# Optimization experiments

Hardware: AMD Instinct MI355X
Metric: run time of the kernel (lower is better)

Reference implementation:

```python
import jax, jax.numpy as jnp
import numpy as np

FEAT = 9
H = 128
L = 2
NH = 4
EPS = 1e-5


def _ln(v, g, b):
    m = v.mean(-1, keepdims=True)
    var = ((v - m) ** 2).mean(-1, keepdims=True)
    return (v - m) * jax.lax.rsqrt(var + EPS) * g + b


def _grn(x, fc1_w, fc1_b, fc2_w, fc2_b, gate_w, gate_b, ln_g, ln_b, skip_w=None, skip_b=None):
    h1 = jax.nn.elu(x @ fc1_w.T + fc1_b)
    h = h1 @ fc2_w.T + fc2_b
    g = jax.nn.sigmoid(h1 @ gate_w.T + gate_b)
    s = x if skip_w is None else x @ skip_w.T + skip_b
    return _ln(s + h * g, ln_g, ln_b)


def _lstm(xs, wih, whh, bih, bhh, h0, c0):
    # xs: [B,T,I]; PyTorch gate order i,f,g,o
    pre = jnp.einsum('bti,gi->btg', xs, wih) + bih  # hoist input projection out of scan

    def step(carry, p):
        h, c = carry
        gates = p + h @ whh.T + bhh
        i, f, g, o = jnp.split(gates, 4, axis=-1)
        c = jax.nn.sigmoid(f) * c + jax.nn.sigmoid(i) * jnp.tanh(g)
        h = jax.nn.sigmoid(o) * jnp.tanh(c)
        return (h, c), h

    (h, c), ys = jax.lax.scan(step, (h0, c0), jnp.swapaxes(pre, 0, 1))
    return jnp.swapaxes(ys, 0, 1), h, c


def _mha(q, k, v, in_w, in_b, out_w, out_b):
    B, Tq, _ = q.shape
    Tk = k.shape[1]
    dh = H // NH
    wq, wk, wv = jnp.split(in_w, 3, axis=0)
    bq, bk, bv = jnp.split(in_b, 3, axis=0)
    Q = (q @ wq.T + bq).reshape(B, Tq, NH, dh)
    K = (k @ wk.T + bk).reshape(B, Tk, NH, dh)
    V = (v @ wv.T + bv).reshape(B, Tk, NH, dh)
    a = jnp.einsum('bqhd,bkhd->bhqk', Q, K) * (dh ** -0.5)
    a = jax.nn.softmax(a, axis=-1)
    o = jnp.einsum('bhqk,bkhd->bqhd', a, V).reshape(B, Tq, H)
    return o @ out_w.T + out_b


def _forward(x, vsn_fc1_w, vsn_fc1_b, vsn_fc2_w, vsn_fc2_b, vsn_gate_w, vsn_gate_b,
             vsn_skip_w, vsn_skip_b, vsn_ln_g, vsn_ln_b,
             gc_fc1_w, gc_fc1_b, gc_fc2_w, gc_fc2_b, gc_gate_w, gc_gate_b,
             gc_skip_w, gc_skip_b, gc_ln_g, gc_ln_b,
             enc_wih, enc_whh, enc_bih, enc_bhh,
             dec_wih, dec_whh, dec_bih, dec_bhh,
             attn_in_w, attn_in_b, attn_out_w, attn_out_b,
             pa_fc1_w, pa_fc1_b, pa_fc2_w, pa_fc2_b, pa_gate_w, pa_gate_b, pa_ln_g, pa_ln_b,
             fo_w, fo_b, encoder_steps, forecast_steps):
    B = x.shape[0]
    # --- VariableSelectionNetwork, batched over (batch * time) instead of per-timestep loop ---
    xe = x[:, :encoder_steps, :].reshape(B * encoder_steps, FEAT)  # [N,9]
    # per-feature GRNs with input_dim=1: fc1 weight is a column vector -> broadcast multiply
    h1 = jax.nn.elu(xe[:, :, None] * vsn_fc1_w[None] + vsn_fc1_b[None])  # [N,9,128]
    h = jnp.einsum('nfi,foi->nfo', h1, vsn_fc2_w) + vsn_fc2_b
    g = jax.nn.sigmoid(jnp.einsum('nfi,foi->nfo', h1, vsn_gate_w) + vsn_gate_b)
    s = xe[:, :, None] * vsn_skip_w[None] + vsn_skip_b[None]
    proc = _ln(s + h * g, vsn_ln_g, vsn_ln_b)  # [N,9,128]
    sel = _grn(proc.reshape(-1, FEAT * H), gc_fc1_w, gc_fc1_b, gc_fc2_w, gc_fc2_b,
               gc_gate_w, gc_gate_b, gc_ln_g, gc_ln_b, gc_skip_w, gc_skip_b)  # [N,128]
    enc_in = sel.reshape(B, encoder_steps, H)
    # --- 2-layer encoder LSTM ---
    z = jnp.zeros((B, H), x.dtype)
    y = enc_in
    hs, cs = [], []
    for l in range(L):
        y, hh, cc = _lstm(y, enc_wih[l], enc_whh[l], enc_bih[l], enc_bhh[l], z, z)
        hs.append(hh)
        cs.append(cc)
    enc_out = y  # [B,168,128]
    # --- decoder: last encoder output repeated, init state from encoder ---
    dec_in = jnp.repeat(enc_out[:, -1:, :], forecast_steps, axis=1)
    y = dec_in
    for l in range(L):
        y, _, _ = _lstm(y, dec_wih[l], dec_whh[l], dec_bih[l], dec_bhh[l], hs[l], cs[l])
    # --- cross attention decoder -> encoder ---
    attn = _mha(y, enc_out, enc_out, attn_in_w, attn_in_b, attn_out_w, attn_out_b)
    a = _grn(attn.reshape(-1, H), pa_fc1_w, pa_fc1_b, pa_fc2_w, pa_fc2_b,
             pa_gate_w, pa_gate_b, pa_ln_g, pa_ln_b)
    a = a.reshape(B, forecast_steps, H)
    return a @ fo_w.T + fo_b  # [B,24,6] (6 per-output linears fused)


def setup_inputs() -> dict:
    key = jax.random.key(0)
    ks = iter(jax.random.split(key, 64))

    def rn(*s):
        return jax.random.normal(next(ks), s, dtype=jnp.float32) * 0.05

    B = 256
    return dict(
        x=jax.random.normal(next(ks), (B, 168, FEAT), dtype=jnp.float32),
        vsn_fc1_w=rn(FEAT, H), vsn_fc1_b=rn(FEAT, H),
        vsn_fc2_w=rn(FEAT, H, H), vsn_fc2_b=rn(FEAT, H),
        vsn_gate_w=rn(FEAT, H, H), vsn_gate_b=rn(FEAT, H),
        vsn_skip_w=rn(FEAT, H), vsn_skip_b=rn(FEAT, H),
        vsn_ln_g=jnp.ones((FEAT, H), jnp.float32), vsn_ln_b=jnp.zeros((FEAT, H), jnp.float32),
        gc_fc1_w=rn(H, FEAT * H), gc_fc1_b=rn(H),
        gc_fc2_w=rn(H, H), gc_fc2_b=rn(H),
        gc_gate_w=rn(H, H), gc_gate_b=rn(H),
        gc_skip_w=rn(H, FEAT * H), gc_skip_b=rn(H),
        gc_ln_g=jnp.ones((H,), jnp.float32), gc_ln_b=jnp.zeros((H,), jnp.float32),
        enc_wih=rn(L, 4 * H, H), enc_whh=rn(L, 4 * H, H), enc_bih=rn(L, 4 * H), enc_bhh=rn(L, 4 * H),
        dec_wih=rn(L, 4 * H, H), dec_whh=rn(L, 4 * H, H), dec_bih=rn(L, 4 * H), dec_bhh=rn(L, 4 * H),
        attn_in_w=rn(3 * H, H), attn_in_b=rn(3 * H),
        attn_out_w=rn(H, H), attn_out_b=rn(H),
        pa_fc1_w=rn(H, H), pa_fc1_b=rn(H),
        pa_fc2_w=rn(H, H), pa_fc2_b=rn(H),
        pa_gate_w=rn(H, H), pa_gate_b=rn(H),
        pa_ln_g=jnp.ones((H,), jnp.float32), pa_ln_b=jnp.zeros((H,), jnp.float32),
        fo_w=rn(6, H), fo_b=rn(6),
        encoder_steps=168, forecast_steps=24,
    )


def reference(x, vsn_fc1_w, vsn_fc1_b, vsn_fc2_w, vsn_fc2_b, vsn_gate_w, vsn_gate_b,
              vsn_skip_w, vsn_skip_b, vsn_ln_g, vsn_ln_b,
              gc_fc1_w, gc_fc1_b, gc_fc2_w, gc_fc2_b, gc_gate_w, gc_gate_b,
              gc_skip_w, gc_skip_b, gc_ln_g, gc_ln_b,
              enc_wih, enc_whh, enc_bih, enc_bhh,
              dec_wih, dec_whh, dec_bih, dec_bhh,
              attn_in_w, attn_in_b, attn_out_w, attn_out_b,
              pa_fc1_w, pa_fc1_b, pa_fc2_w, pa_fc2_b, pa_gate_w, pa_gate_b, pa_ln_g, pa_ln_b,
              fo_w, fo_b, encoder_steps, forecast_steps):
    return _forward(x, vsn_fc1_w, vsn_fc1_b, vsn_fc2_w, vsn_fc2_b, vsn_gate_w, vsn_gate_b,
                    vsn_skip_w, vsn_skip_b, vsn_ln_g, vsn_ln_b,
                    gc_fc1_w, gc_fc1_b, gc_fc2_w, gc_fc2_b, gc_gate_w, gc_gate_b,
                    gc_skip_w, gc_skip_b, gc_ln_g, gc_ln_b,
                    enc_wih, enc_whh, enc_bih, enc_bhh,
                    dec_wih, dec_whh, dec_bih, dec_bhh,
                    attn_in_w, attn_in_b, attn_out_w, attn_out_b,
                    pa_fc1_w, pa_fc1_b, pa_fc2_w, pa_fc2_b, pa_gate_w, pa_gate_b, pa_ln_g, pa_ln_b,
                    fo_w, fo_b, encoder_steps, forecast_steps)
```

## Files before the change

### kernel.cpp

```cpp
#include <hip/hip_runtime.h>
#include <hip/hip_bf16.h>

#define NBATCH 256
#define TSE 168
#define TSD 24
#define NTOK (NBATCH*TSE)
#define NDTOK (NBATCH*TSD)

#define PK_VSN    0
#define PK_GC1    294912
#define PK_GC2    589824
#define PK_ENC0   622592
#define PK_ENC1   688128
#define PK_DEC0   753664
#define PK_DEC1   819200
#define PK_AIN    884736
#define PK_AOUT   933888
#define PK_PAF1   950272
#define PK_PAF2G  966656

typedef __attribute__((ext_vector_type(8))) short short8;
typedef __attribute__((ext_vector_type(4))) float f32x4;
typedef __attribute__((ext_vector_type(2))) __fp16 fp16x2;

__device__ __forceinline__ float sigm(float x){ return 1.f/(1.f + __expf(-x)); }
__device__ __forceinline__ float tanhx(float x){
  float cx = fminf(fmaxf(x, -15.f), 15.f);
  float e = __expf(2.f*cx);
  return (e-1.f)/(e+1.f);
}
__device__ __forceinline__ float eluf(float x){ return x > 0.f ? x : (__expf(x)-1.f); }
__device__ __forceinline__ unsigned short f2bu(float v){
  unsigned int u = __float_as_uint(v);
  u = (u + 0x7fffu + ((u>>16)&1u)) >> 16;
  return (unsigned short)u;
}
__device__ __forceinline__ unsigned int pkh(float a, float b){
  union { fp16x2 h; unsigned int u; } v;
  v.h = __builtin_amdgcn_cvt_pkrtz(a, b);
  return v.u;
}
__device__ __forceinline__ unsigned short f2h(float x){
  union { _Float16 h; unsigned short u; } v;
  v.h = (_Float16)x; return v.u;
}
__device__ __forceinline__ float h2f(unsigned short u){
  union { unsigned short u; _Float16 h; } v;
  v.u = u; return (float)v.h;
}
__device__ __forceinline__ float fd2(unsigned int a, unsigned int b, float c){
  union { unsigned int u; fp16x2 h; } ua, ub;
  ua.u = a; ub.u = b;
  return __builtin_amdgcn_fdot2(ua.h, ub.h, c, false);
}

__global__ __launch_bounds__(256) void k_pack(
    const float* __restrict__ s0, const float* __restrict__ s1,
    unsigned short* __restrict__ dst, int K, int NC, int nsplit,
    int s0bs, int s1bs, int dstbs)
{
  int id = blockIdx.x*256 + threadIdx.x;
  if (id >= K*NC) return;
  int by = blockIdx.y;
  int n = id / K, k = id - n*K;
  float v = (n < nsplit) ? s0[(size_t)by*s0bs + (size_t)n*K + k]
                         : s1[(size_t)by*s1bs + (size_t)(n-nsplit)*K + k];
  int ct = n >> 4, kc = k >> 5;
  int lane = (n & 15) | (((k >> 3) & 3) << 4);
  int j = k & 7;
  int KC = K >> 5;
  dst[(size_t)by*dstbs + (((size_t)ct*KC + kc)*64 + lane)*8 + j] = f2bu(v);
}

__global__ __launch_bounds__(256) void k_vsn_mfma(
    const float* __restrict__ x, const float* __restrict__ fc1_w, const float* __restrict__ fc1_b,
    const unsigned short* __restrict__ pk, const float* __restrict__ fc2_b,
    const float* __restrict__ gate_b, const float* __restrict__ skip_w,
    const float* __restrict__ skip_b, const float* __restrict__ ln_g,
    const float* __restrict__ ln_b, unsigned short* __restrict__ proc2)
{
  const int f = blockIdx.y;
  const int nb = blockIdx.x;
  const int n0 = nb * 64;
  const int tid = threadIdx.x;
  const int wv = tid >> 6, l = tid & 63;
  __shared__ __align__(16) unsigned short As[64*136];
  __shared__ float xs[64];
  __shared__ float vbuf[64*129];
  __shared__ float red[64][4][2];
  __shared__ float mr[64][2];
  if (tid < 64) xs[tid] = x[(size_t)(n0+tid)*9 + f];
  __syncthreads();
  { int i = tid & 127;
    float w1 = fc1_w[f*128 + i], b1 = fc1_b[f*128 + i];
    for (int it = 0; it < 32; it++) {
      int tk = (tid >> 7) + it*2;
      As[tk*136 + i] = f2bu(eluf(xs[tk]*w1 + b1));
    }
  }
  __syncthreads();
  const unsigned short* Wp = pk + PK_VSN + (size_t)f*32768;
  f32x4 acc[4][4];
  #pragma unroll
  for (int rt = 0; rt < 4; rt++)
    #pragma unroll
    for (int ci = 0; ci < 4; ci++) acc[rt][ci] = (f32x4)(0.f);
  #pragma unroll
  for (int kc = 0; kc < 4; kc++) {
    short8 af[4];
    #pragma unroll
    for (int rt = 0; rt < 4; rt++) {
      int row = rt*16 + (l & 15), g = kc*4 + (l >> 4);
      af[rt] = *(const short8*)&As[row*136 + g*8];
    }
    short8 bf[4];
    #pragma unroll
    for (int ci = 0; ci < 4; ci++) {
      int ct = (ci < 2) ? (wv*2 + ci) : (8 + wv*2 + (ci-2));
      bf[ci] = *(const short8*)&Wp[(((size_t)ct*4 + kc)*64 + l)*8];
    }
    #pragma unroll
    for (int rt = 0; rt < 4; rt++)
      #pragma unroll
      for (int ci = 0; ci < 4; ci++)
        acc[rt][ci] = __builtin_amdgcn_mfma_f32_16x16x32_bf16(af[rt], bf[ci], acc[rt][ci], 0, 0, 0);
  }
  __syncthreads();
  #pragma unroll
  for (int ci = 0; ci < 2; ci++) {
    int ch = wv*32 + ci*16 + (l & 15);
    float fb = fc2_b[f*128 + ch], gb = gate_b[f*128 + ch];
    float sw = skip_w[f*128 + ch], sb = skip_b[f*128 + ch];
    #pragma unroll
    for (int rt = 0; rt < 4; rt++)
      #pragma unroll
      for (int r = 0; r < 4; r++) {
        int row = rt*16 + (l >> 4)*4 + r;
        float hv = acc[rt][ci][r] + fb;
        float gv = sigm(acc[rt][ci+2][r] + gb);
        float sv = xs[row]*sw + sb;
        vbuf[row*129 + ch] = sv + hv*gv;
      }
  }
  __syncthreads();
  { int tk = tid >> 2, q = tid & 3;
    float s1 = 0.f, s2 = 0.f;
    #pragma unroll
    for (int i = 0; i < 32; i++) { float z = vbuf[tk*129 + q*32 + i]; s1 += z; s2 += z*z; }
    red[tk][q][0] = s1; red[tk][q][1] = s2;
  }
  __syncthreads();
  if ((tid & 3) == 0) {
    int tk = tid >> 2;
    float a = 0.f, b2 = 0.f;
    for (int p = 0; p < 4; p++) { a += red[tk][p][0]; b2 += red[tk][p][1]; }
    float mean = a * 0.0078125f;
    float var = b2 * 0.0078125f - mean*mean;
    mr[tk][0] = mean; mr[tk][1] = rsqrtf(fmaxf(var, 0.f) + 1e-5f);
  }
  __syncthreads();
  { int i = tid & 127;
    float lg = ln_g[f*128 + i], lb = ln_b[f*128 + i];
    size_t base = ((size_t)nb*9 + f)*8192;
    for (int it = 0; it < 32; it++) {
      int tk = (tid >> 7) + it*2;
      float z = (vbuf[tk*129 + i] - mr[tk][0]) * mr[tk][1] * lg + lb;
      proc2[base + tk*128 + i] = f2bu(z);
    }
  }
}

__global__ __launch_bounds__(256) void k_gc_mfma(
    const unsigned short* __restrict__ proc2, const unsigned short* __restrict__ pk,
    const float* __restrict__ fc1_b, const float* __restrict__ fc2_b,
    const float* __restrict__ gate_b, const float* __restrict__ skip_b,
    const float* __restrict__ ln_g, const float* __restrict__ ln_b,
    unsigned short* __restrict__ selb)
{
  const int nb = blockIdx.x;
  const int n0 = nb * 64;
  const int tid = threadIdx.x;
  const int wv = tid >> 6, l = tid & 63;
  __shared__ __align__(16) unsigned short As[64*136];
  __shared__ __align__(16) unsigned short A2s[64*136];
  __shared__ float vbuf[64*129];
  __shared__ float red[64][4][2];
  __shared__ float mr[64][2];
  const unsigned short* W1 = pk + PK_GC1;
  f32x4 acc1[4][4];
  #pragma unroll
  for (int rt = 0; rt < 4; rt++)
    #pragma unroll
    for (int ci = 0; ci < 4; ci++) acc1[rt][ci] = (f32x4)(0.f);
  for (int c = 0; c < 9; c++) {
    size_t cbase = ((size_t)nb*9 + c)*8192;
    #pragma unroll
    for (int i = 0; i < 4; i++) {
      int gi = i*256 + tid;
      int row = gi >> 4, g = gi & 15;
      uint4 v = *(const uint4*)(proc2 + cbase + row*128 + g*8);
      *(uint4*)&As[row*136 + g*8] = v;
    }
    __syncthreads();
    #pragma unroll
    for (int kc = 0; kc < 4; kc++) {
      int kk = c*4 + kc;
      short8 af[4];
      #pragma unroll
      for (int rt = 0; rt < 4; rt++) {
        int row = rt*16 + (l & 15), g = kc*4 + (l >> 4);
        af[rt] = *(const short8*)&As[row*136 + g*8];
      }
      short8 bf[4];
      #pragma unroll
      for (int ci = 0; ci < 4; ci++) {
        int ct = (ci < 2) ? (wv*2 + ci) : (8 + wv*2 + (ci-2));
        bf[ci] = *(const short8*)&W1[(((size_t)ct*36 + kk)*64 + l)*8];
      }
      #pragma unroll
      for (int rt = 0; rt < 4; rt++)
        #pragma unroll
        for (int ci = 0; ci < 4; ci++)
          acc1[rt][ci] = __builtin_amdgcn_mfma_f32_16x16x32_bf16(af[rt], bf[ci], acc1[rt][ci], 0, 0, 0);
    }
    __syncthreads();
  }
  #pragma unroll
  for (int ci = 0; ci < 2; ci++) {
    int ch = wv*32 + ci*16 + (l & 15);
    float fb = fc1_b[ch];
    #pragma unroll
    for (int rt = 0; rt < 4; rt++)
      #pragma unroll
      for (int r = 0; r < 4; r++) {
        int row = rt*16 + (l >> 4)*4 + r;
        A2s[row*136 + ch] = f2bu(eluf(acc1[rt][ci][r] + fb));
      }
  }
  __syncthreads();
  const unsigned short* W2 = pk + PK_GC2;
  f32x4 acc2[4][4];
  #pragma unroll
  for (int rt = 0; rt < 4; rt++)
    #pragma unroll
    for (int ci = 0; ci < 4; ci++) acc2[rt][ci] = (f32x4)(0.f);
  #pragma unroll
  for (int kc = 0; kc < 4; kc++) {
    short8 af[4];
    #pragma unroll
    for (int rt = 0; rt < 4; rt++) {
      int row = rt*16 + (l & 15), g = kc*4 + (l >> 4);
      af[rt] = *(const short8*)&A2s[row*136 + g*8];
    }
    short8 bf[4];
    #pragma unroll
    for (int ci = 0; ci < 4; ci++) {
      int ct = (ci < 2) ? (wv*2 + ci) : (8 + wv*2 + (ci-2));
      bf[ci] = *(const short8*)&W2[(((size_t)ct*4 + kc)*64 + l)*8];
    }
    #pragma unroll
    for (int rt = 0; rt < 4; rt++)
      #pragma unroll
      for (int ci = 0; ci < 4; ci++)
        acc2[rt][ci] = __builtin_amdgcn_mfma_f32_16x16x32_bf16(af[rt], bf[ci], acc2[rt][ci], 0, 0, 0);
  }
  __syncthreads();
  #pragma unroll
  for (int ci = 0; ci < 2; ci++) {
    int ch = wv*32 + ci*16 + (l & 15);
    float f2 = fc2_b[ch], gb = gate_b[ch], sb = skip_b[ch];
    #pragma unroll
    for (int rt = 0; rt < 4; rt++)
      #pragma unroll
      for (int r = 0; r < 4; r++) {
        int row = rt*16 + (l >> 4)*4 + r;
        float hv = acc2[rt][ci][r] + f2;
        float gv = sigm(acc2[rt][ci+2][r] + gb);
        float sv = acc1[rt][ci+2][r] + sb;
        vbuf[row*129 + ch] = sv + hv*gv;
      }
  }
  __syncthreads();
  { int tk = tid >> 2, q = tid & 3;
    float s1 = 0.f, s2 = 0.f;
    #pragma unroll
    for (int i = 0; i < 32; i++) { float z = vbuf[tk*129 + q*32 + i]; s1 += z; s2 += z*z; }
    red[tk][q][0] = s1; red[tk][q][1] = s2;
  }
  __syncthreads();
  if ((tid & 3) == 0) {
    int tk = tid >> 2;
    float a = 0.f, b2 = 0.f;
    for (int p = 0; p < 4; p++) { a += red[tk][p][0]; b2 += red[tk][p][1]; }
    float mean = a * 0.0078125f;
    float var = b2 * 0.0078125f - mean*mean;
    mr[tk][0] = mean; mr[tk][1] = rsqrtf(fmaxf(var, 0.f) + 1e-5f);
  }
  __syncthreads();
  { int i = tid & 127;
    float lg = ln_g[i], lb = ln_b[i];
    for (int it = 0; it < 32; it++) {
      int tk = (tid >> 7) + it*2;
      float z = (vbuf[tk*129 + i] - mr[tk][0]) * mr[tk][1] * lg + lb;
      selb[(size_t)(n0+tk)*128 + i] = f2bu(z);
    }
  }
}

__global__ __launch_bounds__(256) void k_mm(
    const unsigned short* __restrict__ A, const unsigned short* __restrict__ Wp,
    const float* __restrict__ b0, const float* __restrict__ b1,
    void* __restrict__ out, int out_ld, int outmode)
{
  const int r0 = blockIdx.x * 64;
  const int cb = blockIdx.y * 128;
  const int tid = threadIdx.x;
  const int wv = tid >> 6, l = tid & 63;
  __shared__ __align__(16) unsigned short As[64*136];
  #pragma unroll
  for (int i = 0; i < 4; i++) {
    int gi = i*256 + tid;
    int row = gi >> 4, g = gi & 15;
    uint4 v = *(const uint4*)(A + (size_t)(r0+row)*128 + g*8);
    *(uint4*)&As[row*136 + g*8] = v;
  }
  __syncthreads();
  f32x4 acc[4][2];
  #pragma unroll
  for (int rt = 0; rt < 4; rt++)
    #pragma unroll
    for (int ci = 0; ci < 2; ci++) acc[rt][ci] = (f32x4)(0.f);
  #pragma unroll
  for (int kc = 0; kc < 4; kc++) {
    short8 af[4];
    #pragma unroll
    for (int rt = 0; rt < 4; rt++) {
      int row = rt*16 + (l & 15), g = kc*4 + (l >> 4);
      af[rt] = *(const short8*)&As[row*136 + g*8];
    }
    short8 bf[2];
    #pragma unroll
    for (int ci = 0; ci < 2; ci++) {
      int ct = (cb >> 4) + wv*2 + ci;
      bf[ci] = *(const short8*)&Wp[(((size_t)ct*4 + kc)*64 + l)*8];
    }
    #pragma unroll
    for (int rt = 0; rt < 4; rt++)
      #pragma unroll
      for (int ci = 0; ci < 2; ci++)
        acc[rt][ci] = __builtin_amdgcn_mfma_f32_16x16x32_bf16(af[rt], bf[ci], acc[rt][ci], 0, 0, 0);
  }
  #pragma unroll
  for (int ci = 0; ci < 2; ci++) {
    int cl = cb + wv*32 + ci*16 + (l & 15);
    float bias = b0[cl] + (b1 ? b1[cl] : 0.f);
    #pragma unroll
    for (int rt = 0; rt < 4; rt++)
      #pragma unroll
      for (int r = 0; r < 4; r++) {
        int row = r0 + rt*16 + (l >> 4)*4 + r;
        float v = acc[rt][ci][r] + bias;
        if (outmode == 0) ((float*)out)[(size_t)row*out_ld + cl] = v;
        else ((unsigned short*)out)[(size_t)row*out_ld + cl] = f2h(v);
      }
  }
}

__global__ __launch_bounds__(512, 1) void k_lscan(
    const unsigned short* __restrict__ pre,
    const float* __restrict__ whh,
    const float* __restrict__ h0i, const float* __restrict__ c0i,
    int T, int tstr,
    unsigned short* __restrict__ ys,
    float* __restrict__ hT, float* __restrict__ cT,
    unsigned short* __restrict__ hTb)
{
  const int b = blockIdx.x, tid = threadIdx.x;
  unsigned int w[64];
  {
    const float* p0 = whh + (size_t)tid*128;
    #pragma unroll
    for (int k = 0; k < 64; k++) w[k] = pkh(p0[2*k], p0[2*k+1]);
  }
  __shared__ __align__(16) unsigned short hs[128];
  __shared__ float fg[512];
  float c = 0.f;
  if (tid < 128) {
    float h = h0i ? h0i[(size_t)b*128 + tid] : 0.f;
    c = c0i ? c0i[(size_t)b*128 + tid] : 0.f;
    hs[tid] = f2h(h);
  }
  __syncthreads();
  const unsigned short* preb = pre + (size_t)b * (tstr ? (size_t)T*tstr : 512);
  for (int t = 0; t < T; t++) {
    unsigned short p = preb[(size_t)t*tstr + tid];
    float a0 = 0.f, a1 = 0.f, a2 = 0.f, a3 = 0.f;
    #pragma unroll
    for (int k4 = 0; k4 < 16; k4++) {
      uint4 hh = *(const uint4*)&hs[k4*8];
      a0 = fd2(w[4*k4+0], hh.x, a0);
      a1 = fd2(w[4*k4+1], hh.y, a1);
      a2 = fd2(w[4*k4+2], hh.z, a2);
      a3 = fd2(w[4*k4+3], hh.w, a3);
    }
    fg[tid] = h2f(p) + (a0+a1) + (a2+a3);
    __syncthreads();
    if (tid < 128) {
      float iv = sigm (fg[tid]);
      float fv = sigm (fg[128 + tid]);
      float gv = tanhx(fg[256 + tid]);
      float ov = sigm (fg[384 + tid]);
      c = fv*c + iv*gv;
      float h = ov * tanhx(c);
      hs[tid] = f2h(h);
      ys[((size_t)b*T + t)*128 + tid] = f2bu(h);
      if (t == T-1) {
        hT[(size_t)b*128 + tid] = h;
        cT[(size_t)b*128 + tid] = c;
        hTb[(size_t)b*128 + tid] = f2bu(h);
      }
    }
    __syncthreads();
  }
}

__global__ __launch_bounds__(256) void k_attn(
    const float* __restrict__ Q, const float* __restrict__ K, const float* __restrict__ V,
    unsigned short* __restrict__ o)
{
  const int b = blockIdx.x, h = blockIdx.y, tid = threadIdx.x;
  __shared__ float Ks[168][33];
  __shared__ float Vs[168][32];
  __shared__ float Qs[24][32];
  __shared__ float Sc[24][169];
  __shared__ float red[24][8];
  __shared__ float rowm[24], rows[24];
  for (int e = tid; e < 168*32; e += 256) {
    int t = e >> 5, d = e & 31;
    Ks[t][d] = K[((size_t)b*168 + t)*128 + h*32 + d];
    Vs[t][d] = V[((size_t)b*168 + t)*128 + h*32 + d];
  }
  for (int e = tid; e < 24*32; e += 256) {
    int q = e >> 5, d = e & 31;
    Qs[q][d] = Q[((size_t)b*24 + q)*128 + h*32 + d];
  }
  __syncthreads();
  for (int e = tid; e < 24*168; e += 256) {
    int q = e / 168, t = e - q*168;
    float s = 0.f;
    #pragma unroll
    for (int d = 0; d < 32; d++) s += Qs[q][d]*Ks[t][d];
    Sc[q][t] = s * 0.17677669529663687f;
  }
  __syncthreads();
  int q = tid >> 3, l8 = tid & 7;
  if (q < 24) {
    float m = -1e30f;
    for (int t = l8; t < 168; t += 8) m = fmaxf(m, Sc[q][t]);
    red[q][l8] = m;
  }
  __syncthreads();
  if (q < 24 && l8 == 0) {
    float m = red[q][0];
    for (int p = 1; p < 8; p++) m = fmaxf(m, red[q][p]);
    rowm[q] = m;
  }
  __syncthreads();
  if (q < 24) {
    float s = 0.f;
    for (int t = l8; t < 168; t += 8) {
      float e2 = __expf(Sc[q][t] - rowm[q]);
      Sc[q][t] = e2; s += e2;
    }
    red[q][l8] = s;
  }
  __syncthreads();
  if (q < 24 && l8 == 0) {
    float s = 0.f;
    for (int p = 0; p < 8; p++) s += red[q][p];
    rows[q] = 1.f/s;
  }
  __syncthreads();
  for (int e = tid; e < 24*32; e += 256) {
    int qq = e >> 5, d = e & 31;
    float acc = 0.f;
    for (int t = 0; t < 168; t++) acc += Sc[qq][t]*Vs[t][d];
    o[((size_t)b*24 + qq)*128 + h*32 + d] = f2bu(acc * rows[qq]);
  }
}

__global__ __launch_bounds__(256) void k_pa_mfma(
    const float* __restrict__ xin, const unsigned short* __restrict__ pk,
    const float* __restrict__ fc1_b, const float* __restrict__ fc2_b,
    const float* __restrict__ gate_b, const float* __restrict__ ln_g,
    const float* __restrict__ ln_b, float* __restrict__ out)
{
  const int n0 = blockIdx.x * 64;
  const int tid = threadIdx.x;
  const int wv = tid >> 6, l = tid & 63;
  __shared__ __align__(16) unsigned short As[64*136];
  __shared__ __align__(16) unsigned short A2s[64*136];
  __shared__ float xs[64*129];
  __shared__ float red[64][4][2];
  __shared__ float mr[64][2];
  for (int i2 = 0; i2 < 8; i2++) {
    int t4 = i2*256 + tid;
    int r = t4 >> 5, cc = (t4 & 31) << 2;
    float4 v = *(const float4*)(xin + (size_t)(n0 + r)*128 + cc);
    xs[r*129 + cc] = v.x; xs[r*129 + cc+1] = v.y;
    xs[r*129 + cc+2] = v.z; xs[r*129 + cc+3] = v.w;
    As[r*136 + cc] = f2bu(v.x); As[r*136 + cc+1] = f2bu(v.y);
    As[r*136 + cc+2] = f2bu(v.z); As[r*136 + cc+3] = f2bu(v.w);
  }
  __syncthreads();
  const unsigned short* W1 = pk + PK_PAF1;
  f32x4 acc1[4][2];
  #pragma unroll
  for (int rt = 0; rt < 4; rt++)
    #pragma unroll
    for (int ci = 0; ci < 2; ci++) acc1[rt][ci] = (f32x4)(0.f);
  #pragma unroll
  for (int kc = 0; kc < 4; kc++) {
    short8 af[4];
    #pragma unroll
    for (int rt = 0; rt < 4; rt++) {
      int row = rt*16 + (l & 15), g = kc*4 + (l >> 4);
      af[rt] = *(const short8*)&As[row*136 + g*8];
    }
    short8 bf[2];
    #pragma unroll
    for (int ci = 0; ci < 2; ci++) {
      int ct = wv*2 + ci;
      bf[ci] = *(const short8*)&W1[(((size_t)ct*4 + kc)*64 + l)*8];
    }
    #pragma unroll
    for (int rt = 0; rt < 4; rt++)
      #pragma unroll
      for (int ci = 0; ci < 2; ci++)
        acc1[rt][ci] = __builtin_amdgcn_mfma_f32_16x16x32_bf16(af[rt], bf[ci], acc1[rt][ci], 0, 0, 0);
  }
  __syncthreads();
  #pragma unroll
  for (int ci = 0; ci < 2; ci++) {
    int ch = wv*32 + ci*16 + (l & 15);
    float fb = fc1_b[ch];
    #pragma unroll
    for (int rt = 0; rt < 4; rt++)
      #pragma unroll
      for (int r = 0; r < 4; r++) {
        int row = rt*16 + (l >> 4)*4 + r;
        A2s[row*136 + ch] = f2bu(eluf(acc1[rt][ci][r] + fb));
      }
  }
  __syncthreads();
  const unsigned short* W2 = pk + PK_PAF2G;
  f32x4 acc2[4][4];
  #pragma unroll
  for (int rt = 0; rt < 4; rt++)
    #pragma unroll
    for (int ci = 0; ci < 4; ci++) acc2[rt][ci] = (f32x4)(0.f);
  #pragma unroll
  for (int kc = 0; kc < 4; kc++) {
    short8 af[4];
    #pragma unroll
    for (int rt = 0; rt < 4; rt++) {
      int row = rt*16 + (l & 15), g = kc*4 + (l >> 4);
      af[rt] = *(const short8*)&A2s[row*136 + g*8];
    }
    short8 bf[4];
    #pragma unroll
    for (int ci = 0; ci < 4; ci++) {
      int ct = (ci < 2) ? (wv*2 + ci) : (8 + wv*2 + (ci-2));
      bf[ci] = *(const short8*)&W2[(((size_t)ct*4 + kc)*64 + l)*8];
    }
    #pragma unroll
    for (int rt = 0; rt < 4; rt++)
      #pragma unroll
      for (int ci = 0; ci < 4; ci++)
        acc2[rt][ci] = __builtin_amdgcn_mfma_f32_16x16x32_bf16(af[rt], bf[ci], acc2[rt][ci], 0, 0, 0);
  }
  __syncthreads();
  #pragma unroll
  for (int ci = 0; ci < 2; ci++) {
    int ch = wv*32 + ci*16 + (l & 15);
    float f2 = fc2_b[ch], gb = gate_b[ch];
    #pragma unroll
    for (int rt = 0; rt < 4; rt++)
      #pragma unroll
      for (int r = 0; r < 4; r++) {
        int row = rt*16 + (l >> 4)*4 + r;
        float hv = acc2[rt][ci][r] + f2;
        float gv = sigm(acc2[rt][ci+2][r] + gb);
        xs[row*129 + ch] = xs[row*129 + ch] + hv*gv;
      }
  }
  __syncthreads();
  { int tk = tid >> 2, q = tid & 3;
    float s1 = 0.f, s2 = 0.f;
    #pragma unroll
    for (int i = 0; i < 32; i++) { float z = xs[tk*129 + q*32 + i]; s1 += z; s2 += z*z; }
    red[tk][q][0] = s1; red[tk][q][1] = s2;
  }
  __syncthreads();
  if ((tid & 3) == 0) {
    int tk = tid >> 2;
    float a = 0.f, b2 = 0.f;
    for (int p = 0; p < 4; p++) { a += red[tk][p][0]; b2 += red[tk][p][1]; }
    float mean = a * 0.0078125f;
    float var = b2 * 0.0078125f - mean*mean;
    mr[tk][0] = mean; mr[tk][1] = rsqrtf(fmaxf(var, 0.f) + 1e-5f);
  }
  __syncthreads();
  { int i = tid & 127;
    float lg = ln_g[i], lb = ln_b[i];
    for (int it = 0; it < 32; it++) {
      int tk = (tid >> 7) + it*2;
      out[(size_t)(n0+tk)*128 + i] = (xs[tk*129 + i] - mr[tk][0]) * mr[tk][1] * lg + lb;
    }
  }
}

__global__ __launch_bounds__(256) void k_final(
    const float* __restrict__ a, const float* __restrict__ fo_w,
    const float* __restrict__ fo_b, float* __restrict__ out)
{
  int idx = blockIdx.x*256 + threadIdx.x;
  if (idx >= NDTOK*6) return;
  int n = idx / 6, j = idx - n*6;
  const float* ar = a + (size_t)n*128;
  const float* w = fo_w + j*128;
  float s = fo_b[j];
  #pragma unroll 4
  for (int d = 0; d < 128; d++) s += ar[d]*w[d];
  out[idx] = s;
}

extern "C" void kernel_launch(void* const* d_in, const int* in_sizes, int n_in,
                              void* d_out, int out_size, void* d_ws, size_t ws_size,
                              hipStream_t stream) {
  (void)in_sizes; (void)n_in; (void)out_size; (void)ws_size;
  const float* x      = (const float*)d_in[0];
  const float* vfc1w  = (const float*)d_in[1];
  const float* vfc1b  = (const float*)d_in[2];
  const float* vfc2w  = (const float*)d_in[3];
  const float* vfc2b  = (const float*)d_in[4];
  const float* vgw    = (const float*)d_in[5];
  const float* vgb    = (const float*)d_in[6];
  const float* vskw   = (const float*)d_in[7];
  const float* vskb   = (const float*)d_in[8];
  const float* vlng   = (const float*)d_in[9];
  const float* vlnb   = (const float*)d_in[10];
  const float* gfc1w  = (const float*)d_in[11];
  const float* gfc1b  = (const float*)d_in[12];
  const float* gfc2w  = (const float*)d_in[13];
  const float* gfc2b  = (const float*)d_in[14];
  const float* ggw    = (const float*)d_in[15];
  const float* ggb    = (const float*)d_in[16];
  const float* gskw   = (const float*)d_in[17];
  const float* gskb   = (const float*)d_in[18];
  const float* glng   = (const float*)d_in[19];
  const float* glnb   = (const float*)d_in[20];
  const float* encwih = (const float*)d_in[21];
  const float* encwhh = (const float*)d_in[22];
  const float* encbih = (const float*)d_in[23];
  const float* encbhh = (const float*)d_in[24];
  const float* decwih = (const float*)d_in[25];
  const float* decwhh = (const float*)d_in[26];
  const float* decbih = (const float*)d_in[27];
  const float* decbhh = (const float*)d_in[28];
  const float* ainw   = (const float*)d_in[29];
  const float* ainb   = (const float*)d_in[30];
  const float* aoutw  = (const float*)d_in[31];
  const float* aoutb  = (const float*)d_in[32];
  const float* pfc1w  = (const float*)d_in[33];
  const float* pfc1b  = (const float*)d_in[34];
  const float* pfc2w  = (const float*)d_in[35];
  const float* pfc2b  = (const float*)d_in[36];
  const float* pgw    = (const float*)d_in[37];
  const float* pgb    = (const float*)d_in[38];
  const float* plng   = (const float*)d_in[39];
  const float* plnb   = (const float*)d_in[40];
  const float* fow    = (const float*)d_in[41];
  const float* fob    = (const float*)d_in[42];

  float* ws = (float*)d_ws;
  unsigned short* pk = (unsigned short*)ws;
  unsigned short* proc2 = (unsigned short*)(ws + 530000);
  unsigned short* pre = (unsigned short*)(ws + 530000);
  float* Kb   = ws + 530000;
  float* Vb   = ws + 6100000;
  unsigned short* pre2 = (unsigned short*)(ws + 11700000);
  float* Qb   = ws + 13300000;
  unsigned short* attb = (unsigned short*)(ws + 14100000);
  float* ato  = ws + 14300000;
  float* pao  = ws + 15100000;
  unsigned short* pd0 = (unsigned short*)(ws + 15900000);
  unsigned short* selb  = (unsigned short*)(ws + 25350000);
  unsigned short* encob = (unsigned short*)(ws + 28150000);
  unsigned short* ys0b  = (unsigned short*)(ws + 30950000);
  unsigned short* dys0b = (unsigned short*)(ws + 33750000);
  unsigned short* dout2b = (unsigned short*)(ws + 33950000);
  float* hT0  = ws + 34150000;  float* cT0 = ws + 34190000;
  float* hT1  = ws + 34230000;  float* cT1 = ws + 34270000;
  unsigned short* hT1b = (unsigned short*)(ws + 34310000);
  float* dscr = ws + 34350000;

  k_pack<<<dim3(128, 9), dim3(256), 0, stream>>>(vfc2w, vgw, pk + PK_VSN, 128, 256, 128, 16384, 16384, 32768);
  k_pack<<<dim3(1152), dim3(256), 0, stream>>>(gfc1w, gskw, pk + PK_GC1, 1152, 256, 128, 0, 0, 0);
  k_pack<<<dim3(128), dim3(256), 0, stream>>>(gfc2w, ggw, pk + PK_GC2, 128, 256, 128, 0, 0, 0);
  k_pack<<<dim3(256), dim3(256), 0, stream>>>(encwih, encwih, pk + PK_ENC0, 128, 512, 512, 0, 0, 0);
  k_pack<<<dim3(256), dim3(256), 0, stream>>>(encwih + 65536, encwih, pk + PK_ENC1, 128, 512, 512, 0, 0, 0);
  k_pack<<<dim3(256), dim3(256), 0, stream>>>(decwih, decwih, pk + PK_DEC0, 128, 512, 512, 0, 0, 0);
  k_pack<<<dim3(256), dim3(256), 0, stream>>>(decwih + 65536, decwih, pk + PK_DEC1, 128, 512, 512, 0, 0, 0);
  k_pack<<<dim3(192), dim3(256), 0, stream>>>(ainw, ainw, pk + PK_AIN, 128, 384, 384, 0, 0, 0);
  k_pack<<<dim3(64), dim3(256), 0, stream>>>(aoutw, aoutw, pk + PK_AOUT, 128, 128, 128, 0, 0, 0);
  k_pack<<<dim3(64), dim3(256), 0, stream>>>(pfc1w, pfc1w, pk + PK_PAF1, 128, 128, 128, 0, 0, 0);
  k_pack<<<dim3(128), dim3(256), 0, stream>>>(pfc2w, pgw, pk + PK_PAF2G, 128, 256, 128, 0, 0, 0);
  k_vsn_mfma<<<dim3(672, 9), dim3(256), 0, stream>>>(x, vfc1w, vfc1b, pk,
      vfc2b, vgb, vskw, vskb, vlng, vlnb, proc2);
  k_gc_mfma<<<dim3(672), dim3(256), 0, stream>>>(proc2, pk, gfc1b, gfc2b, ggb,
      gskb, glng, glnb, selb);
  k_mm<<<dim3(672, 4), dim3(256), 0, stream>>>(selb, pk + PK_ENC0, encbih, encbhh, pre, 512, 1);
  k_lscan<<<dim3(256), dim3(512), 0, stream>>>(pre, encwhh, nullptr, nullptr,
      TSE, 512, ys0b, hT0, cT0, (unsigned short*)dscr);
  k_mm<<<dim3(672, 4), dim3(256), 0, stream>>>(ys0b, pk + PK_ENC1, encbih + 512, encbhh + 512, pre, 512, 1);
  k_lscan<<<dim3(256), dim3(512), 0, stream>>>(pre, encwhh + 65536, nullptr, nullptr,
      TSE, 512, encob, hT1, cT1, hT1b);
  k_mm<<<dim3(4, 4), dim3(256), 0, stream>>>(hT1b, pk + PK_DEC0, decbih, decbhh, pd0, 512, 1);
  k_lscan<<<dim3(256), dim3(512), 0, stream>>>(pd0, decwhh, hT0, cT0,
      TSD, 0, dys0b, dscr + 40000, dscr + 80000, (unsigned short*)dscr);
  k_mm<<<dim3(96, 4), dim3(256), 0, stream>>>(dys0b, pk + PK_DEC1, decbih + 512, decbhh + 512, pre2, 512, 1);
  k_lscan<<<dim3(256), dim3(512), 0, stream>>>(pre2, decwhh + 65536, hT1, cT1,
      TSD, 512, dout2b, dscr + 120000, dscr + 160000, (unsigned short*)dscr);
  k_mm<<<dim3(96, 1), dim3(256), 0, stream>>>(dout2b, pk + PK_AIN, ainb, nullptr, Qb, 128, 0);
  k_mm<<<dim3(672, 1), dim3(256), 0, stream>>>(encob, pk + PK_AIN + 16384, ainb + 128, nullptr, Kb, 128, 0);
  k_mm<<<dim3(672, 1), dim3(256), 0, stream>>>(encob, pk + PK_AIN + 32768, ainb + 256, nullptr, Vb, 128, 0);
  k_attn<<<dim3(256, 4), dim3(256), 0, stream>>>(Qb, Kb, Vb, attb);
  k_mm<<<dim3(96, 1), dim3(256), 0, stream>>>(attb, pk + PK_AOUT, aoutb, nullptr, ato, 128, 0);
  k_pa_mfma<<<dim3(96), dim3(256), 0, stream>>>(ato, pk, pfc1b, pfc2b, pgb,
      plng, plnb, pao);
  k_final<<<dim3(144), dim3(256), 0, stream>>>(pao, fow, fob, (float*)d_out);
}
```

Baseline: 739.1 us.

## Batch LSTM recurrence over 16 sequences per block using MFMA

Replaces the per-sequence LSTM scan, which ran fp16 dot2 products with one block per batch element, with an MFMA scan in which each block handles 16 batch rows and keeps the packed bf16 recurrent weights in registers. The input-projection GEMM now writes its output in the MFMA accumulator fragment layout, so each lane can load its precomputed gate inputs directly. New pack launches prepare the Whh weights. This cuts the grid from 256 blocks to 16, trading parallelism for tensor-core throughput and fewer synchronisations per step. The hidden state is also rounded to bf16 instead of fp16, which lowers precision.

```diff
diff --git a/kernel.cpp b/kernel.cpp
--- a/kernel.cpp
+++ b/kernel.cpp
@@ -18,6 +18,10 @@
 #define PK_AOUT   933888
 #define PK_PAF1   950272
 #define PK_PAF2G  966656
+#define PK_WHH_E0 999424
+#define PK_WHH_E1 1064960
+#define PK_WHH_D0 1130496
+#define PK_WHH_D1 1196032
 
 typedef __attribute__((ext_vector_type(8))) short short8;
 typedef __attribute__((ext_vector_type(4))) float f32x4;
@@ -35,11 +39,6 @@
   u = (u + 0x7fffu + ((u>>16)&1u)) >> 16;
   return (unsigned short)u;
 }
-__device__ __forceinline__ unsigned int pkh(float a, float b){
-  union { fp16x2 h; unsigned int u; } v;
-  v.h = __builtin_amdgcn_cvt_pkrtz(a, b);
-  return v.u;
-}
 __device__ __forceinline__ unsigned short f2h(float x){
   union { _Float16 h; unsigned short u; } v;
   v.h = (_Float16)x; return v.u;
@@ -47,11 +46,6 @@
 __device__ __forceinline__ float h2f(unsigned short u){
   union { unsigned short u; _Float16 h; } v;
   v.u = u; return (float)v.h;
-}
-__device__ __forceinline__ float fd2(unsigned int a, unsigned int b, float c){
-  union { unsigned int u; fp16x2 h; } ua, ub;
-  ua.u = a; ub.u = b;
-  return __builtin_amdgcn_fdot2(ua.h, ub.h, c, false);
 }
 
 __global__ __launch_bounds__(256) void k_pack(
@@ -310,7 +304,7 @@
 __global__ __launch_bounds__(256) void k_mm(
     const unsigned short* __restrict__ A, const unsigned short* __restrict__ Wp,
     const float* __restrict__ b0, const float* __restrict__ b1,
-    void* __restrict__ out, int out_ld, int outmode)
+    void* __restrict__ out, int out_ld, int outmode, int Tt)
 {
   const int r0 = blockIdx.x * 64;
   const int cb = blockIdx.y * 128;
@@ -361,66 +355,123 @@
         int row = r0 + rt*16 + (l >> 4)*4 + r;
         float v = acc[rt][ci][r] + bias;
         if (outmode == 0) ((float*)out)[(size_t)row*out_ld + cl] = v;
-        else ((unsigned short*)out)[(size_t)row*out_ld + cl] = f2h(v);
-      }
-  }
-}
-
-__global__ __launch_bounds__(512, 1) void k_lscan(
-    const unsigned short* __restrict__ pre,
-    const float* __restrict__ whh,
+        else if (outmode == 1) ((unsigned short*)out)[(size_t)row*out_ld + cl] = f2h(v);
+        else {
+          int bb = row / Tt, tt = row - bb*Tt;
+          int tile = cl >> 4;
+          int l2 = (cl & 15) | (((bb >> 2) & 3) << 4);
+          int r2 = bb & 3;
+          ((unsigned short*)out)[((((size_t)(bb >> 4)*Tt + tt)*32 + tile)*64 + l2)*4 + r2] = f2h(v);
+        }
+      }
+  }
+}
+
+__global__ __launch_bounds__(256, 1) void k_lscan_mfma(
+    const unsigned short* __restrict__ prep,
+    const unsigned short* __restrict__ Wp,
     const float* __restrict__ h0i, const float* __restrict__ c0i,
-    int T, int tstr,
+    int T, int Tt,
     unsigned short* __restrict__ ys,
     float* __restrict__ hT, float* __restrict__ cT,
     unsigned short* __restrict__ hTb)
 {
-  const int b = blockIdx.x, tid = threadIdx.x;
-  unsigned int w[64];
-  {
-    const float* p0 = whh + (size_t)tid*128;
-    #pragma unroll
-    for (int k = 0; k < 64; k++) w[k] = pkh(p0[2*k], p0[2*k+1]);
-  }
-  __shared__ __align__(16) unsigned short hs[128];
-  __shared__ float fg[512];
-  float c = 0.f;
-  if (tid < 128) {
-    float h = h0i ? h0i[(size_t)b*128 + tid] : 0.f;
-    c = c0i ? c0i[(size_t)b*128 + tid] : 0.f;
-    hs[tid] = f2h(h);
-  }
-  __syncthreads();
-  const unsigned short* preb = pre + (size_t)b * (tstr ? (size_t)T*tstr : 512);
+  const int blk = blockIdx.x, tid = threadIdx.x;
+  const int wv = tid >> 6, l = tid & 63;
+  const int b0 = blk * 16;
+  const int q = l >> 4, cl = l & 15;
+  short8 bfr[4][2][4];
+  #pragma unroll
+  for (int g = 0; g < 4; g++)
+    #pragma unroll
+    for (int gr = 0; gr < 2; gr++) {
+      int ct = g*8 + wv + gr*4;
+      #pragma unroll
+      for (int kc = 0; kc < 4; kc++)
+        bfr[g][gr][kc] = *(const short8*)&Wp[(((size_t)ct*4 + kc)*64 + l)*8];
+    }
+  __shared__ __align__(16) unsigned short hA[2][16*136];
+  #pragma unroll
+  for (int i = 0; i < 8; i++) {
+    int e = i*256 + tid;
+    int m = e >> 7, k = e & 127;
+    float h = h0i ? h0i[(size_t)(b0+m)*128 + k] : 0.f;
+    hA[0][m*136 + k] = f2bu(h);
+  }
+  float cst[2][4];
+  #pragma unroll
+  for (int gr = 0; gr < 2; gr++) {
+    int ch = (wv + gr*4)*16 + cl;
+    #pragma unroll
+    for (int r = 0; r < 4; r++) {
+      int m = q*4 + r;
+      cst[gr][r] = c0i ? c0i[(size_t)(b0+m)*128 + ch] : 0.f;
+    }
+  }
+  __syncthreads();
+  int cur = 0;
   for (int t = 0; t < T; t++) {
-    unsigned short p = preb[(size_t)t*tstr + tid];
-    float a0 = 0.f, a1 = 0.f, a2 = 0.f, a3 = 0.f;
-    #pragma unroll
-    for (int k4 = 0; k4 < 16; k4++) {
-      uint4 hh = *(const uint4*)&hs[k4*8];
-      a0 = fd2(w[4*k4+0], hh.x, a0);
-      a1 = fd2(w[4*k4+1], hh.y, a1);
-      a2 = fd2(w[4*k4+2], hh.z, a2);
-      a3 = fd2(w[4*k4+3], hh.w, a3);
-    }
-    fg[tid] = h2f(p) + (a0+a1) + (a2+a3);
+    unsigned int pu[4][2][2];
+    {
+      int tu = (Tt == 1) ? 0 : t;
+      const unsigned short* pb = prep + ((size_t)blk*Tt + tu)*8192;
+      #pragma unroll
+      for (int g = 0; g < 4; g++)
+        #pragma unroll
+        for (int gr = 0; gr < 2; gr++) {
+          int tile = g*8 + wv + gr*4;
+          const unsigned short* pp = pb + ((size_t)tile*64 + l)*4;
+          pu[g][gr][0] = *(const unsigned int*)pp;
+          pu[g][gr][1] = *(const unsigned int*)(pp + 2);
+        }
+    }
+    short8 af[4];
+    #pragma unroll
+    for (int kc = 0; kc < 4; kc++)
+      af[kc] = *(const short8*)&hA[cur][cl*136 + (kc*4 + q)*8];
+    f32x4 acc[4][2];
+    #pragma unroll
+    for (int g = 0; g < 4; g++)
+      #pragma unroll
+      for (int gr = 0; gr < 2; gr++) {
+        f32x4 a = (f32x4)(0.f);
+        #pragma unroll
+        for (int kc = 0; kc < 4; kc++)
+          a = __builtin_amdgcn_mfma_f32_16x16x32_bf16(af[kc], bfr[g][gr][kc], a, 0, 0, 0);
+        acc[g][gr] = a;
+      }
+    int nxt = cur ^ 1;
+    #pragma unroll
+    for (int gr = 0; gr < 2; gr++) {
+      int ch = (wv + gr*4)*16 + cl;
+      #pragma unroll
+      for (int r = 0; r < 4; r++) {
+        unsigned int ui = pu[0][gr][r >> 1], uf = pu[1][gr][r >> 1];
+        unsigned int ug = pu[2][gr][r >> 1], uo = pu[3][gr][r >> 1];
+        float pi = h2f((unsigned short)((r & 1) ? (ui >> 16) : (ui & 0xffff)));
+        float pf = h2f((unsigned short)((r & 1) ? (uf >> 16) : (uf & 0xffff)));
+        float pg = h2f((unsigned short)((r & 1) ? (ug >> 16) : (ug & 0xffff)));
+        float po = h2f((unsigned short)((r & 1) ? (uo >> 16) : (uo & 0xffff)));
+        float gi = sigm (acc[0][gr][r] + pi);
+        float gf = sigm (acc[1][gr][r] + pf);
+        float gg = tanhx(acc[2][gr][r] + pg);
+        float go = sigm (acc[3][gr][r] + po);
+        float c2 = gf*cst[gr][r] + gi*gg;
+        cst[gr][r] = c2;
+        float h = go * tanhx(c2);
+        int m = q*4 + r;
+        unsigned short hb = f2bu(h);
+        hA[nxt][m*136 + ch] = hb;
+        ys[((size_t)(b0+m)*T + t)*128 + ch] = hb;
+        if (t == T-1) {
+          hT[(size_t)(b0+m)*128 + ch] = h;
+          cT[(size_t)(b0+m)*128 + ch] = c2;
+          hTb[(size_t)(b0+m)*128 + ch] = hb;
+        }
+      }
+    }
     __syncthreads();
-    if (tid < 128) {
-      float iv = sigm (fg[tid]);
-      float fv = sigm (fg[128 + tid]);
-      float gv = tanhx(fg[256 + tid]);
-      float ov = sigm (fg[384 + tid]);
-      c = fv*c + iv*gv;
-      float h = ov * tanhx(c);
-      hs[tid] = f2h(h);
-      ys[((size_t)b*T + t)*128 + tid] = f2bu(h);
-      if (t == T-1) {
-        hT[(size_t)b*128 + tid] = h;
-        cT[(size_t)b*128 + tid] = c;
-        hTb[(size_t)b*128 + tid] = f2bu(h);
-      }
-    }
-    __syncthreads();
+    cur = nxt;
   }
 }
 
@@ -685,25 +736,25 @@
 
   float* ws = (float*)d_ws;
   unsigned short* pk = (unsigned short*)ws;
-  unsigned short* proc2 = (unsigned short*)(ws + 530000);
-  unsigned short* pre = (unsigned short*)(ws + 530000);
-  float* Kb   = ws + 530000;
-  float* Vb   = ws + 6100000;
-  unsigned short* pre2 = (unsigned short*)(ws + 11700000);
-  float* Qb   = ws + 13300000;
-  unsigned short* attb = (unsigned short*)(ws + 14100000);
-  float* ato  = ws + 14300000;
-  float* pao  = ws + 15100000;
-  unsigned short* pd0 = (unsigned short*)(ws + 15900000);
-  unsigned short* selb  = (unsigned short*)(ws + 25350000);
-  unsigned short* encob = (unsigned short*)(ws + 28150000);
-  unsigned short* ys0b  = (unsigned short*)(ws + 30950000);
-  unsigned short* dys0b = (unsigned short*)(ws + 33750000);
-  unsigned short* dout2b = (unsigned short*)(ws + 33950000);
-  float* hT0  = ws + 34150000;  float* cT0 = ws + 34190000;
-  float* hT1  = ws + 34230000;  float* cT1 = ws + 34270000;
-  unsigned short* hT1b = (unsigned short*)(ws + 34310000);
-  float* dscr = ws + 34350000;
+  unsigned short* proc2 = (unsigned short*)(ws + 650000);
+  unsigned short* prep  = (unsigned short*)(ws + 650000);
+  float* Kb   = ws + 650000;
+  float* Vb   = ws + 6200000;
+  unsigned short* pre2p = (unsigned short*)(ws + 12000000);
+  unsigned short* pd0p  = (unsigned short*)(ws + 13600000);
+  float* Qb   = ws + 13700000;
+  unsigned short* attb = (unsigned short*)(ws + 14500000);
+  float* ato  = ws + 14800000;
+  float* pao  = ws + 15700000;
+  unsigned short* selb  = (unsigned short*)(ws + 25450000);
+  unsigned short* encob = (unsigned short*)(ws + 28250000);
+  unsigned short* ys0b  = (unsigned short*)(ws + 31050000);
+  unsigned short* dys0b = (unsigned short*)(ws + 33850000);
+  unsigned short* dout2b = (unsigned short*)(ws + 34050000);
+  float* hT0  = ws + 34250000;  float* cT0 = ws + 34290000;
+  float* hT1  = ws + 34330000;  float* cT1 = ws + 34370000;
+  unsigned short* hT1b = (unsigned short*)(ws + 34410000);
+  float* dscr = ws + 34450000;
 
   k_pack<<<dim3(128, 9), dim3(256), 0, stream>>>(vfc2w, vgw, pk + PK_VSN, 128, 256, 128, 16384, 16384, 32768);
   k_pack<<<dim3(1152), dim3(256), 0, stream>>>(gfc1w, gskw, pk + PK_GC1, 1152, 256, 128, 0, 0, 0);
@@ -716,27 +767,31 @@
   k_pack<<<dim3(64), dim3(256), 0, stream>>>(aoutw, aoutw, pk + PK_AOUT, 128, 128, 128, 0, 0, 0);
   k_pack<<<dim3(64), dim3(256), 0, stream>>>(pfc1w, pfc1w, pk + PK_PAF1, 128, 128, 128, 0, 0, 0);
   k_pack<<<dim3(128), dim3(256), 0, stream>>>(pfc2w, pgw, pk + PK_PAF2G, 128, 256, 128, 0, 0, 0);
+  k_pack<<<dim3(256), dim3(256), 0, stream>>>(encwhh, encwhh, pk + PK_WHH_E0, 128, 512, 512, 0, 0, 0);
+  k_pack<<<dim3(256), dim3(256), 0, stream>>>(encwhh + 65536, encwhh, pk + PK_WHH_E1, 128, 512, 512, 0, 0, 0);
+  k_pack<<<dim3(256), dim3(256), 0, stream>>>(decwhh, decwhh, pk + PK_WHH_D0, 128, 512, 512, 0, 0, 0);
+  k_pack<<<dim3(256), dim3(256), 0, stream>>>(decwhh + 65536, decwhh, pk + PK_WHH_D1, 128, 512, 512, 0, 0, 0);
   k_vsn_mfma<<<dim3(672, 9), dim3(256), 0, stream>>>(x, vfc1w, vfc1b, pk,
       vfc2b, vgb, vskw, vskb, vlng, vlnb, proc2);
   k_gc_mfma<<<dim3(672), dim3(256), 0, stream>>>(proc2, pk, gfc1b, gfc2b, ggb,
       gskb, glng, glnb, selb);
-  k_mm<<<dim3(672, 4), dim3(256), 0, stream>>>(selb, pk + PK_ENC0, encbih, encbhh, pre, 512, 1);
-  k_lscan<<<dim3(256), dim3(512), 0, stream>>>(pre, encwhh, nullptr, nullptr,
-      TSE, 512, ys0b, hT0, cT0, (unsigned short*)dscr);
-  k_mm<<<dim3(672, 4), dim3(256), 0, stream>>>(ys0b, pk + PK_ENC1, encbih + 512, encbhh + 512, pre, 512, 1);
-  k_lscan<<<dim3(256), dim3(512), 0, stream>>>(pre, encwhh + 65536, nullptr, nullptr,
-      TSE, 512, encob, hT1, cT1, hT1b);
-  k_mm<<<dim3(4, 4), dim3(256), 0, stream>>>(hT1b, pk + PK_DEC0, decbih, decbhh, pd0, 512, 1);
-  k_lscan<<<dim3(256), dim3(512), 0, stream>>>(pd0, decwhh, hT0, cT0,
-      TSD, 0, dys0b, dscr + 40000, dscr + 80000, (unsigned short*)dscr);
-  k_mm<<<dim3(96, 4), dim3(256), 0, stream>>>(dys0b, pk + PK_DEC1, decbih + 512, decbhh + 512, pre2, 512, 1);
-  k_lscan<<<dim3(256), dim3(512), 0, stream>>>(pre2, decwhh + 65536, hT1, cT1,
-      TSD, 512, dout2b, dscr + 120000, dscr + 160000, (unsigned short*)dscr);
-  k_mm<<<dim3(96, 1), dim3(256), 0, stream>>>(dout2b, pk + PK_AIN, ainb, nullptr, Qb, 128, 0);
-  k_mm<<<dim3(672, 1), dim3(256), 0, stream>>>(encob, pk + PK_AIN + 16384, ainb + 128, nullptr, Kb, 128, 0);
-  k_mm<<<dim3(672, 1), dim3(256), 0, stream>>>(encob, pk + PK_AIN + 32768, ainb + 256, nullptr, Vb, 128, 0);
+  k_mm<<<dim3(672, 4), dim3(256), 0, stream>>>(selb, pk + PK_ENC0, encbih, encbhh, prep, 512, 2, TSE);
+  k_lscan_mfma<<<dim3(16), dim3(256), 0, stream>>>(prep, pk + PK_WHH_E0, nullptr, nullptr,
+      TSE, TSE, ys0b, hT0, cT0, (unsigned short*)dscr);
+  k_mm<<<dim3(672, 4), dim3(256), 0, stream>>>(ys0b, pk + PK_ENC1, encbih + 512, encbhh + 512, prep, 512, 2, TSE);
+  k_lscan_mfma<<<dim3(16), dim3(256), 0, stream>>>(prep, pk + PK_WHH_E1, nullptr, nullptr,
+      TSE, TSE, encob, hT1, cT1, hT1b);
+  k_mm<<<dim3(4, 4), dim3(256), 0, stream>>>(hT1b, pk + PK_DEC0, decbih, decbhh, pd0p, 512, 2, 1);
+  k_lscan_mfma<<<dim3(16), dim3(256), 0, stream>>>(pd0p, pk + PK_WHH_D0, hT0, cT0,
+      TSD, 1, dys0b, dscr + 40000, dscr + 80000, (unsigned short*)dscr);
+  k_mm<<<dim3(96, 4), dim3(256), 0, stream>>>(dys0b, pk + PK_DEC1, decbih + 512, decbhh + 512, pre2p, 512, 2, TSD);
+  k_lscan_mfma<<<dim3(16), dim3(256), 0, stream>>>(pre2p, pk + PK_WHH_D1, hT1, cT1,
+      TSD, TSD, dout2b, dscr + 120000, dscr + 160000, (unsigned short*)dscr);
+  k_mm<<<dim3(96, 1), dim3(256), 0, stream>>>(dout2b, pk + PK_AIN, ainb, nullptr, Qb, 128, 0, 0);
+  k_mm<<<dim3(672, 1), dim3(256), 0, stream>>>(encob, pk + PK_AIN + 16384, ainb + 128, nullptr, Kb, 128, 0, 0);
+  k_mm<<<dim3(672, 1), dim3(256), 0, stream>>>(encob, pk + PK_AIN + 32768, ainb + 256, nullptr, Vb, 128, 0, 0);
   k_attn<<<dim3(256, 4), dim3(256), 0, stream>>>(Qb, Kb, Vb, attb);
-  k_mm<<<dim3(96, 1), dim3(256), 0, stream>>>(attb, pk + PK_AOUT, aoutb, nullptr, ato, 128, 0);
+  k_mm<<<dim3(96, 1), dim3(256), 0, stream>>>(attb, pk + PK_AOUT, aoutb, nullptr, ato, 128, 0, 0);
   k_pa_mfma<<<dim3(96), dim3(256), 0, stream>>>(ato, pk, pfc1b, pfc2b, pgb,
       plng, plnb, pao);
   k_final<<<dim3(144), dim3(256), 0, stream>>>(pao, fow, fob, (float*)d_out);
```

Measured after the change: 1.383 ms. +87.2%, slower.
